# Optimization experiments

Hardware: AMD Instinct MI355X
Metric: run time of the kernel (lower is better)

## Reference

```python
import jax, jax.numpy as jnp
import numpy as np

NUM_EXPERTS = 8
TOP_K = 2


def setup_inputs() -> dict:
    key = jax.random.key(0)
    k0, k1, k2, k3, k4 = jax.random.split(key, 5)
    sl, bs, hs, ffn = 2048, 2, 512, 2048
    T = sl * bs
    x = jax.random.normal(k0, (sl, bs, hs), jnp.float32)
    expert_weights = jax.random.uniform(k1, (T, TOP_K), jnp.float32)
    expert_indices = jax.random.randint(k2, (T, TOP_K), 0, NUM_EXPERTS)
    # per-expert MLP params (ParallelGroupedMLP, 'regular' mlp_type)
    w1 = jax.random.normal(k3, (NUM_EXPERTS, hs, ffn), jnp.float32) * (hs ** -0.5)
    w2 = jax.random.normal(k4, (NUM_EXPERTS, ffn, hs), jnp.float32) * (ffn ** -0.5)
    return dict(x=x, expert_weights=expert_weights, expert_indices=expert_indices, w1=w1, w2=w2)


def reference(x, expert_weights, expert_indices, w1, w2):
    """Dropless MoE: sort assignments by expert, gather tokens, grouped MLP,
    scatter-combine with top-k router weights (megablocks gather/scatter semantics)."""
    in_shape = x.shape
    hs = in_shape[-1]
    x_flat = x.reshape(-1, hs)                 # [T, hs]
    T = x_flat.shape[0]
    flat_ids = expert_indices.reshape(-1)      # [T*k] expert id per assignment
    order = jnp.argsort(flat_ids)              # indices: assignment order sorted by expert
    bin_ids = flat_ids[order]                  # expert id per sorted slot
    token_ids = order // TOP_K                 # source token per sorted slot
    xg = x_flat[token_ids]                     # gather: [T*k, hs]
    # grouped GEMM: fixed small loop over experts, mask-select per slot
    y = jnp.zeros_like(xg)
    for e in range(NUM_EXPERTS):
        h = jax.nn.gelu(xg @ w1[e], approximate=False)   # [T*k, ffn]
        y = jnp.where((bin_ids == e)[:, None], h @ w2[e], y)
    # scatter-combine: out[token] += weight[assignment] * y[slot]
    w = expert_weights.reshape(-1)[order][:, None]       # [T*k, 1]
    out = jnp.zeros((T, hs), x.dtype).at[token_ids].add(w * y)
    return out.reshape(in_shape)
```

## Files before the change

kernel.cpp:

```cpp
#include <hip/hip_runtime.h>
#include <stdint.h>

#define T_TOK 4096
#define KTOP  2
#define HS    512
#define FFN   2048
#define NE    8
#define NA    (T_TOK*KTOP)
#define MT    128
#define BK    64
#define MT_MAX 72
#define SLOT_CAP (MT_MAX*MT)
#define PSTR 68
#define CPAD 32

#define MB_ (1024ull*1024ull)
#define WS_CNT2  0u
#define WS_OFF   1024u
#define WS_MEXP  1088u
#define WS_SLOTS 2048u
#define WS_INV   40960u
#define WS_XB   (1*MB_)
#define WS_W1T  (5*MB_)
#define WS_W2T  (21*MB_)
#define WS_HB   (37*MB_)
#define WS_YPB0 (73*MB_)
#define WS_YPB1 (82*MB_)
#define WS_NEED (91*MB_)

typedef short bf16x8 __attribute__((ext_vector_type(8)));
typedef float f32x4  __attribute__((ext_vector_type(4)));

__device__ __forceinline__ unsigned short f2bf(float f) {
    unsigned u = __builtin_bit_cast(unsigned, f);
    u += 0x7fffu + ((u >> 16) & 1u);
    return (unsigned short)(u >> 16);
}
__device__ __forceinline__ float bf2f(unsigned short h) {
    return __builtin_bit_cast(float, (unsigned)h << 16);
}
__device__ __forceinline__ float gelu_fast(float x) {
    float x2 = x * x;
    float inner = fmaf(0.044715f * x2, x, x);
    float E = __expf(1.5957691216057308f * inner);
    return x - x / (1.0f + E);
}
__device__ __forceinline__ void gl_lds16(const void* g, void* l) {
    __builtin_amdgcn_global_load_lds(
        (const __attribute__((address_space(1))) unsigned int*)g,
        (__attribute__((address_space(3))) unsigned int*)l, 16, 0, 0);
}

__device__ __forceinline__ void transpose_cvt_body(
    const float* __restrict__ src, unsigned short* __restrict__ dh,
    int R, int C, int e, int kb, int nb, int t, float (*tile)[33])
{
    const int k0 = kb * 32, n0 = nb * 32;
    #pragma unroll
    for (int q = 0; q < 4; ++q) {
        int idx = t + q * 256, kk = idx >> 5, nn = idx & 31;
        tile[kk][nn] = src[((size_t)e * R + k0 + kk) * C + n0 + nn];
    }
    __syncthreads();
    #pragma unroll
    for (int q = 0; q < 4; ++q) {
        int idx = t + q * 256, nn = idx >> 5, kk = idx & 31;
        dh[((size_t)e * C + n0 + nn) * R + k0 + kk] = f2bf(tile[kk][nn]);
    }
}

__global__ void moe_prep(int* slots, int* cnt2,
                         const float* __restrict__ x, unsigned short* __restrict__ xb,
                         const float* __restrict__ w1, unsigned short* __restrict__ w1t,
                         const float* __restrict__ w2, unsigned short* __restrict__ w2t)
{
    __shared__ float tile[32][33];
    const int bid = blockIdx.x, t = threadIdx.x;
    if (bid < 2048) {
        int i = bid * 256 + t;
        float4 v = reinterpret_cast<const float4*>(x)[i];
        uint2 p = { (unsigned)f2bf(v.x) | ((unsigned)f2bf(v.y) << 16),
                    (unsigned)f2bf(v.z) | ((unsigned)f2bf(v.w) << 16) };
        reinterpret_cast<uint2*>(xb)[i] = p;
    } else if (bid < 10240) {
        int lin = bid - 2048, e = lin >> 10, rem = lin & 1023;
        transpose_cvt_body(w1, w1t, HS, FFN, e, rem & 15, rem >> 4, t, tile);
    } else if (bid < 18432) {
        int lin = bid - 10240, e = lin >> 10, rem = lin & 1023;
        transpose_cvt_body(w2, w2t, FFN, HS, e, rem & 63, rem >> 6, t, tile);
    } else {
        int gid = (bid - 18432) * 256 + t;
        if (gid < SLOT_CAP) slots[gid] = -1;
        if (gid < NE * CPAD) cnt2[gid] = 0;
    }
}

__global__ void moe_fill(const int* __restrict__ eidx, int* cnt2, int* slots, int* inv,
                         int* offp, int* mexp) {
    __shared__ int h[NE];
    __shared__ int hloc[NE];
    __shared__ int bl[NE];
    __shared__ int off_l[NE + 1];
    const int t = threadIdx.x;
    if (t < NE) { h[t] = 0; hloc[t] = 0; }
    __syncthreads();
    for (int a2 = t; a2 < NA; a2 += 256) atomicAdd(&h[eidx[a2]], 1);
    const int a = blockIdx.x * 256 + t;
    const int e = eidx[a];
    const int rank = atomicAdd(&hloc[e], 1);
    __syncthreads();
    if (t == 0) {
        int run = 0;
        for (int q = 0; q < NE; ++q) { off_l[q] = run; run += ((h[q] + MT - 1) / MT) * MT; }
        off_l[NE] = run;
    }
    __syncthreads();
    if (t < NE) bl[t] = atomicAdd(&cnt2[t * CPAD], hloc[t]);
    if (blockIdx.x == 0) {
        if (t <= NE) offp[t] = off_l[t];
        if (t < MT_MAX) {
            int m0 = t * MT, ee = 0;
            #pragma unroll
            for (int q = 0; q < NE; ++q)
                if (m0 >= off_l[q] && m0 < off_l[q + 1]) ee = q;
            mexp[t] = ee;
        }
    }
    __syncthreads();
    int s = off_l[e] + bl[e] + rank;
    slots[s] = a;
    inv[a] = s;
}

__global__ __launch_bounds__(256, 4) void moe_gemm1(
    const unsigned short* __restrict__ XB, const unsigned short* __restrict__ W1T,
    const int* __restrict__ offp, const int* __restrict__ mexp,
    const int* __restrict__ slots, unsigned short* __restrict__ HB)
{
    const int xcd = blockIdx.x & 7;
    const int part = blockIdx.x >> 3;
    const int mtg = part % 9;
    const int nt  = part / 9;
    const int mt  = xcd * 9 + mtg;
    if (mt * MT >= offp[NE]) return;
    const int e = mexp[mt];
    const int t = threadIdx.x, lane = t & 63, wv = t >> 6;

    __shared__ __align__(16) char POOL[MT * PSTR * 4];
    __shared__ int srow[MT];
    short* As = (short*)POOL;
    short* Bs = (short*)(POOL + 16384);
    float* Pf = (float*)POOL;

    if (t < MT) { int s = slots[mt * MT + t]; srow[t] = (s < 0) ? 0 : (s >> 1); }
    __syncthreads();

    int baseA[4], baseB[4];
    #pragma unroll
    for (int q = 0; q < 4; ++q) {
        int i = wv * 4 + q;
        int row = i * 8 + (lane >> 3);
        int sg = (lane & 7) ^ (row & 7);
        baseA[q] = srow[row] * HS + sg * 8;
        baseB[q] = (e * FFN + nt * MT + row) * HS + sg * 8;
    }

    const int wm = wv >> 1, wn = wv & 1, q4 = lane >> 4, l15 = lane & 15;
    int offA[2][4], offB[2][4];
    #pragma unroll
    for (int m = 0; m < 4; ++m) {
        int r  = wm * 64 + m * 16 + l15;
        int rb = wn * 64 + m * 16 + l15;
        #pragma unroll
        for (int ks = 0; ks < 2; ++ks) {
            offA[ks][m] = r  * 128 + ((((ks << 2) | q4) ^ (r  & 7)) << 4);
            offB[ks][m] = rb * 128 + ((((ks << 2) | q4) ^ (rb & 7)) << 4);
        }
    }

    f32x4 acc[4][4];
    #pragma unroll
    for (int m = 0; m < 4; ++m)
        #pragma unroll
        for (int n = 0; n < 4; ++n) { f32x4 z = {0.f, 0.f, 0.f, 0.f}; acc[m][n] = z; }

    for (int kk = 0; kk < HS; kk += BK) {
        __syncthreads();
        #pragma unroll
        for (int q = 0; q < 4; ++q) {
            int i = wv * 4 + q;
            gl_lds16(XB  + baseA[q] + kk, (char*)As + i * 1024);
            gl_lds16(W1T + baseB[q] + kk, (char*)Bs + i * 1024);
        }
        __syncthreads();
        #pragma unroll
        for (int ks = 0; ks < 2; ++ks) {
            bf16x8 a[4], b[4];
            #pragma unroll
            for (int m = 0; m < 4; ++m) {
                a[m] = *(const bf16x8*)((const char*)As + offA[ks][m]);
                b[m] = *(const bf16x8*)((const char*)Bs + offB[ks][m]);
            }
            #pragma unroll
            for (int m = 0; m < 4; ++m)
                #pragma unroll
                for (int n = 0; n < 4; ++n)
                    acc[m][n] = __builtin_amdgcn_mfma_f32_16x16x32_bf16(a[m], b[n], acc[m][n], 0, 0, 0);
        }
    }

    #pragma unroll
    for (int half = 0; half < 2; ++half) {
        __syncthreads();
        if (wn == half) {
            #pragma unroll
            for (int m = 0; m < 4; ++m)
                #pragma unroll
                for (int n = 0; n < 4; ++n)
                    #pragma unroll
                    for (int j = 0; j < 4; ++j)
                        Pf[(wm * 64 + m * 16 + q4 * 4 + j) * PSTR + n * 16 + l15] = acc[m][n][j];
        }
        __syncthreads();
        #pragma unroll
        for (int q = 0; q < 4; ++q) {
            int seg = q * 256 + t, row = seg >> 3, c8 = (seg & 7) << 3;
            const float* p = Pf + row * PSTR + c8;
            float4 a = *(const float4*)p, b = *(const float4*)(p + 4);
            float va[8] = {a.x, a.y, a.z, a.w, b.x, b.y, b.z, b.w};
            bf16x8 ph;
            #pragma unroll
            for (int i = 0; i < 8; ++i) ph[i] = (short)f2bf(gelu_fast(va[i]));
            *(bf16x8*)(HB + (size_t)(mt * MT + row) * FFN + nt * MT + half * 64 + c8) = ph;
        }
    }
}

__global__ __launch_bounds__(256, 4) void moe_gemm2(
    const unsigned short* __restrict__ HB, const unsigned short* __restrict__ W2T,
    const int* __restrict__ offp, const int* __restrict__ mexp,
    unsigned short* __restrict__ YPB0, unsigned short* __restrict__ YPB1)
{
    const int xcd = blockIdx.x & 7;
    const int part = blockIdx.x >> 3;
    const int mtg = part % 9;
    const int sub = part / 9;
    const int mt  = xcd * 9 + mtg;
    const int nt  = sub >> 1, kpart = sub & 1;
    if (mt * MT >= offp[NE]) return;
    const int e = mexp[mt];
    const int t = threadIdx.x, lane = t & 63, wv = t >> 6;

    __shared__ __align__(16) char POOL[MT * PSTR * 4];
    short* As = (short*)POOL;
    short* Bs = (short*)(POOL + 16384);
    float* Pf = (float*)POOL;

    int baseA[4], baseB[4];
    #pragma unroll
    for (int q = 0; q < 4; ++q) {
        int i = wv * 4 + q;
        int row = i * 8 + (lane >> 3);
        int sg = (lane & 7) ^ (row & 7);
        baseA[q] = (mt * MT + row) * FFN + sg * 8;
        baseB[q] = (e * HS + nt * MT + row) * FFN + sg * 8;
    }

    const int wm = wv >> 1, wn = wv & 1, q4 = lane >> 4, l15 = lane & 15;
    int offA[2][4], offB[2][4];
    #pragma unroll
    for (int m = 0; m < 4; ++m) {
        int r  = wm * 64 + m * 16 + l15;
        int rb = wn * 64 + m * 16 + l15;
        #pragma unroll
        for (int ks = 0; ks < 2; ++ks) {
            offA[ks][m] = r  * 128 + ((((ks << 2) | q4) ^ (r  & 7)) << 4);
            offB[ks][m] = rb * 128 + ((((ks << 2) | q4) ^ (rb & 7)) << 4);
        }
    }

    f32x4 acc[4][4];
    #pragma unroll
    for (int m = 0; m < 4; ++m)
        #pragma unroll
        for (int n = 0; n < 4; ++n) { f32x4 z = {0.f, 0.f, 0.f, 0.f}; acc[m][n] = z; }

    const int k0 = kpart * (FFN / 2), k1 = k0 + FFN / 2;
    for (int kk = k0; kk < k1; kk += BK) {
        __syncthreads();
        #pragma unroll
        for (int q = 0; q < 4; ++q) {
            int i = wv * 4 + q;
            gl_lds16(HB  + baseA[q] + kk, (char*)As + i * 1024);
            gl_lds16(W2T + baseB[q] + kk, (char*)Bs + i * 1024);
        }
        __syncthreads();
        #pragma unroll
        for (int ks = 0; ks < 2; ++ks) {
            bf16x8 a[4], b[4];
            #pragma unroll
            for (int m = 0; m < 4; ++m) {
                a[m] = *(const bf16x8*)((const char*)As + offA[ks][m]);
                b[m] = *(const bf16x8*)((const char*)Bs + offB[ks][m]);
            }
            #pragma unroll
            for (int m = 0; m < 4; ++m)
                #pragma unroll
                for (int n = 0; n < 4; ++n)
                    acc[m][n] = __builtin_amdgcn_mfma_f32_16x16x32_bf16(a[m], b[n], acc[m][n], 0, 0, 0);
        }
    }

    unsigned short* YP = kpart ? YPB1 : YPB0;
    #pragma unroll
    for (int half = 0; half < 2; ++half) {
        __syncthreads();
        if (wn == half) {
            #pragma unroll
            for (int m = 0; m < 4; ++m)
                #pragma unroll
                for (int n = 0; n < 4; ++n)
                    #pragma unroll
                    for (int j = 0; j < 4; ++j)
                        Pf[(wm * 64 + m * 16 + q4 * 4 + j) * PSTR + n * 16 + l15] = acc[m][n][j];
        }
        __syncthreads();
        #pragma unroll
        for (int q = 0; q < 4; ++q) {
            int seg = q * 256 + t, row = seg >> 3, c8 = (seg & 7) << 3;
            const float* p = Pf + row * PSTR + c8;
            float4 a = *(const float4*)p, b = *(const float4*)(p + 4);
            float va[8] = {a.x, a.y, a.z, a.w, b.x, b.y, b.z, b.w};
            bf16x8 ph;
            #pragma unroll
            for (int i = 0; i < 8; ++i) ph[i] = (short)f2bf(va[i]);
            *(bf16x8*)(YP + (size_t)(mt * MT + row) * HS + nt * MT + half * 64 + c8) = ph;
        }
    }
}

__global__ void moe_combine2(const unsigned short* __restrict__ YPB0,
                             const unsigned short* __restrict__ YPB1,
                             const int* __restrict__ inv, const float* __restrict__ ew,
                             float* __restrict__ out) {
    int i = blockIdx.x * 256 + threadIdx.x;
    if (i >= T_TOK * HS / 8) return;
    int tk = i >> 6, c8 = (i & 63) << 3;
    int s0 = inv[2 * tk], s1 = inv[2 * tk + 1];
    float w0 = ew[2 * tk], w1 = ew[2 * tk + 1];
    bf16x8 a0 = *(const bf16x8*)(YPB0 + (size_t)s0 * HS + c8);
    bf16x8 b0 = *(const bf16x8*)(YPB1 + (size_t)s0 * HS + c8);
    bf16x8 a1 = *(const bf16x8*)(YPB0 + (size_t)s1 * HS + c8);
    bf16x8 b1 = *(const bf16x8*)(YPB1 + (size_t)s1 * HS + c8);
    float o[8];
    #pragma unroll
    for (int j = 0; j < 8; ++j)
        o[j] = w0 * (bf2f((unsigned short)a0[j]) + bf2f((unsigned short)b0[j]))
             + w1 * (bf2f((unsigned short)a1[j]) + bf2f((unsigned short)b1[j]));
    float4* d = reinterpret_cast<float4*>(out + (size_t)i * 8);
    d[0] = make_float4(o[0], o[1], o[2], o[3]);
    d[1] = make_float4(o[4], o[5], o[6], o[7]);
}

#define FB_BM 32
#define FB_BJ 128
#define FB_CK 256
#define FB_XSTR (FB_CK+4)
#define FB_HSTR (FB_BJ+4)

__device__ __forceinline__ float fb_gelu(float v) {
    return 0.5f * v * (1.0f + erff(v * 0.70710678118654752f));
}

__global__ void fb_init(int* cnt) { int i = threadIdx.x; if (i < NE) cnt[i] = 0; }

__global__ void fb_scatter(const int* __restrict__ eidx, int* cnt, int* bucket) {
    int a = blockIdx.x * 256 + threadIdx.x;
    if (a < NA) { int e = eidx[a]; int p = atomicAdd(&cnt[e], 1); bucket[e * NA + p] = a; }
}

__global__ __launch_bounds__(256, 1) void fb_fused(
    const float* __restrict__ x, const float* __restrict__ w1, const float* __restrict__ w2,
    const int* __restrict__ cnt, const int* __restrict__ bucket, float* __restrict__ ybuf)
{
    const int bid = blockIdx.x;
    const int e = bid & (NE - 1), tr = bid >> 3;
    const int n_e = cnt[e], rbase = tr * FB_BM;
    if (rbase >= n_e) return;
    const int t = threadIdx.x;
    __shared__ __align__(16) float Xc[FB_BM][FB_XSTR];
    __shared__ __align__(16) float Hsh[FB_BM][FB_HSTR];
    __shared__ int rowa[FB_BM];
    if (t < FB_BM) { int r = rbase + t; rowa[t] = (r < n_e) ? bucket[e * NA + r] : -1; }
    __syncthreads();
    const int cg = t & 15, rg = t >> 4, r0 = rg * 2;
    float yac[2][32];
    #pragma unroll
    for (int u = 0; u < 2; ++u)
        #pragma unroll
        for (int v = 0; v < 32; ++v) yac[u][v] = 0.0f;
    const float* w1e = w1 + (size_t)e * HS * FFN;
    const float* w2e = w2 + (size_t)e * FFN * HS;
    for (int jp = 0; jp < FFN; jp += FB_BJ) {
        float hac[2][8];
        #pragma unroll
        for (int u = 0; u < 2; ++u)
            #pragma unroll
            for (int v = 0; v < 8; ++v) hac[u][v] = 0.0f;
        for (int ic = 0; ic < HS; ic += FB_CK) {
            __syncthreads();
            #pragma unroll
            for (int q = 0; q < (FB_BM * FB_CK / 4) / 256; ++q) {
                int id = t + 256 * q, rr = id >> 6, c4 = id & 63;
                int a = rowa[rr];
                float4 val = make_float4(0.f, 0.f, 0.f, 0.f);
                if (a >= 0) val = *reinterpret_cast<const float4*>(x + (size_t)(a >> 1) * HS + ic + c4 * 4);
                *reinterpret_cast<float4*>(&Xc[rr][c4 * 4]) = val;
            }
            __syncthreads();
            const float* w1p = w1e + (size_t)ic * FFN + jp + cg * 8;
            #pragma unroll 2
            for (int i4 = 0; i4 < FB_CK; i4 += 4) {
                float4 xa = *reinterpret_cast<const float4*>(&Xc[r0][i4]);
                float4 xb = *reinterpret_cast<const float4*>(&Xc[r0 + 1][i4]);
                const float* wr0 = w1p + (size_t)i4 * FFN;
                #pragma unroll
                for (int ii = 0; ii < 4; ++ii) {
                    float4 wa = *reinterpret_cast<const float4*>(wr0 + (size_t)ii * FFN);
                    float4 wb = *reinterpret_cast<const float4*>(wr0 + (size_t)ii * FFN + 4);
                    float x0 = (ii == 0) ? xa.x : (ii == 1) ? xa.y : (ii == 2) ? xa.z : xa.w;
                    float x1 = (ii == 0) ? xb.x : (ii == 1) ? xb.y : (ii == 2) ? xb.z : xb.w;
                    hac[0][0] = fmaf(x0, wa.x, hac[0][0]); hac[0][1] = fmaf(x0, wa.y, hac[0][1]);
                    hac[0][2] = fmaf(x0, wa.z, hac[0][2]); hac[0][3] = fmaf(x0, wa.w, hac[0][3]);
                    hac[0][4] = fmaf(x0, wb.x, hac[0][4]); hac[0][5] = fmaf(x0, wb.y, hac[0][5]);
                    hac[0][6] = fmaf(x0, wb.z, hac[0][6]); hac[0][7] = fmaf(x0, wb.w, hac[0][7]);
                    hac[1][0] = fmaf(x1, wa.x, hac[1][0]); hac[1][1] = fmaf(x1, wa.y, hac[1][1]);
                    hac[1][2] = fmaf(x1, wa.z, hac[1][2]); hac[1][3] = fmaf(x1, wa.w, hac[1][3]);
                    hac[1][4] = fmaf(x1, wb.x, hac[1][4]); hac[1][5] = fmaf(x1, wb.y, hac[1][5]);
                    hac[1][6] = fmaf(x1, wb.z, hac[1][6]); hac[1][7] = fmaf(x1, wb.w, hac[1][7]);
                }
            }
        }
        #pragma unroll
        for (int u = 0; u < 2; ++u)
            #pragma unroll
            for (int v = 0; v < 8; ++v) Hsh[r0 + u][cg * 8 + v] = fb_gelu(hac[u][v]);
        __syncthreads();
        const float* w2p = w2e + (size_t)jp * HS + cg * 32;
        #pragma unroll 2
        for (int j = 0; j < FB_BJ; ++j) {
            float h0 = Hsh[r0][j], h1 = Hsh[r0 + 1][j];
            const float* wr = w2p + (size_t)j * HS;
            #pragma unroll
            for (int q = 0; q < 8; ++q) {
                float4 w4 = *reinterpret_cast<const float4*>(wr + q * 4);
                yac[0][q * 4 + 0] = fmaf(h0, w4.x, yac[0][q * 4 + 0]);
                yac[0][q * 4 + 1] = fmaf(h0, w4.y, yac[0][q * 4 + 1]);
                yac[0][q * 4 + 2] = fmaf(h0, w4.z, yac[0][q * 4 + 2]);
                yac[0][q * 4 + 3] = fmaf(h0, w4.w, yac[0][q * 4 + 3]);
                yac[1][q * 4 + 0] = fmaf(h1, w4.x, yac[1][q * 4 + 0]);
                yac[1][q * 4 + 1] = fmaf(h1, w4.y, yac[1][q * 4 + 1]);
                yac[1][q * 4 + 2] = fmaf(h1, w4.z, yac[1][q * 4 + 2]);
                yac[1][q * 4 + 3] = fmaf(h1, w4.w, yac[1][q * 4 + 3]);
            }
        }
    }
    #pragma unroll
    for (int u = 0; u < 2; ++u) {
        int a = rowa[r0 + u];
        if (a >= 0) {
            float* yp = ybuf + (size_t)a * HS + cg * 32;
            #pragma unroll
            for (int q = 0; q < 8; ++q) {
                float4 o = make_float4(yac[u][q * 4 + 0], yac[u][q * 4 + 1],
                                       yac[u][q * 4 + 2], yac[u][q * 4 + 3]);
                *reinterpret_cast<float4*>(yp + q * 4) = o;
            }
        }
    }
}

__global__ void fb_combine(const float* __restrict__ ybuf, const float* __restrict__ ew,
                           float* __restrict__ out) {
    int i = blockIdx.x * 256 + threadIdx.x;
    if (i >= T_TOK * HS / 4) return;
    int tk = i >> 7, c4 = i & 127;
    float wA = ew[2 * tk], wB = ew[2 * tk + 1];
    const float4* y4 = reinterpret_cast<const float4*>(ybuf);
    float4 a = y4[(size_t)(2 * tk) * (HS / 4) + c4];
    float4 b = y4[(size_t)(2 * tk + 1) * (HS / 4) + c4];
    float4 o;
    o.x = wA * a.x + wB * b.x; o.y = wA * a.y + wB * b.y;
    o.z = wA * a.z + wB * b.z; o.w = wA * a.w + wB * b.w;
    reinterpret_cast<float4*>(out)[i] = o;
}

extern "C" void kernel_launch(void* const* d_in, const int* in_sizes, int n_in,
                              void* d_out, int out_size, void* d_ws, size_t ws_size,
                              hipStream_t stream) {
    const float* x  = (const float*)d_in[0];
    const float* ew = (const float*)d_in[1];
    const int*   ei = (const int*)d_in[2];
    const float* w1 = (const float*)d_in[3];
    const float* w2 = (const float*)d_in[4];
    float* out = (float*)d_out;
    char* W = (char*)d_ws;

    if (ws_size < WS_NEED) {
        int* cnt = (int*)d_ws;
        int* bucket = cnt + 64;
        float* ybuf = (float*)(W + (1 << 19));
        fb_init<<<1, 64, 0, stream>>>(cnt);
        fb_scatter<<<NA / 256, 256, 0, stream>>>(ei, cnt, bucket);
        fb_fused<<<NE * (NA / FB_BM), 256, 0, stream>>>(x, w1, w2, cnt, bucket, ybuf);
        fb_combine<<<(T_TOK * HS / 4 + 255) / 256, 256, 0, stream>>>(ybuf, ew, out);
        return;
    }

    int* cnt2  = (int*)(W + WS_CNT2);
    int* offp  = (int*)(W + WS_OFF);
    int* mexp  = (int*)(W + WS_MEXP);
    int* slots = (int*)(W + WS_SLOTS);
    int* inv   = (int*)(W + WS_INV);
    unsigned short* XB   = (unsigned short*)(W + WS_XB);
    unsigned short* W1T  = (unsigned short*)(W + WS_W1T);
    unsigned short* W2T  = (unsigned short*)(W + WS_W2T);
    unsigned short* HB   = (unsigned short*)(W + WS_HB);
    unsigned short* YPB0 = (unsigned short*)(W + WS_YPB0);
    unsigned short* YPB1 = (unsigned short*)(W + WS_YPB1);

    moe_prep<<<18468, 256, 0, stream>>>(slots, cnt2, x, XB, w1, W1T, w2, W2T);
    moe_fill<<<NA / 256, 256, 0, stream>>>(ei, cnt2, slots, inv, offp, mexp);
    moe_gemm1<<<8 * 9 * 16, 256, 0, stream>>>(XB, W1T, offp, mexp, slots, HB);
    moe_gemm2<<<8 * 9 * 8, 256, 0, stream>>>(HB, W2T, offp, mexp, YPB0, YPB1);
    moe_combine2<<<(T_TOK * HS / 8) / 256, 256, 0, stream>>>(YPB0, YPB1, inv, ew, out);
}
```

Baseline: 101.5 us.

## Fuse routing fill into prep kernel with deterministic prefix-based slot ranks

Merges the separate routing-fill kernel into the prep kernel, so there is one fewer launch and no global atomic counter to zero. Each routing block recomputes the full histogram plus a prefix histogram of all earlier assignments and takes ranks by a linear scan, which makes slot order deterministic. One extra block pads only the unused slots and writes the offsets and expert map. The gemm2 block-to-tile mapping is also reordered so consecutive blocks share the same M tile. The cost is that each of 33 blocks scans all 8192 expert ids and runs an O(t) rank loop.

Result: no change. 101.2 us (-0.2%).

```diff
diff --git a/kernel.cpp b/kernel.cpp
--- a/kernel.cpp
+++ b/kernel.cpp
@@ -12,10 +12,8 @@
 #define MT_MAX 72
 #define SLOT_CAP (MT_MAX*MT)
 #define PSTR 68
-#define CPAD 32
 
 #define MB_ (1024ull*1024ull)
-#define WS_CNT2  0u
 #define WS_OFF   1024u
 #define WS_MEXP  1088u
 #define WS_SLOTS 2048u
@@ -69,7 +67,8 @@
     }
 }
 
-__global__ void moe_prep(int* slots, int* cnt2,
+__global__ void moe_prep(const int* __restrict__ eidx,
+                         int* slots, int* inv, int* offp, int* mexp,
                          const float* __restrict__ x, unsigned short* __restrict__ xb,
                          const float* __restrict__ w1, unsigned short* __restrict__ w1t,
                          const float* __restrict__ w2, unsigned short* __restrict__ w2t)
@@ -89,47 +88,47 @@
         int lin = bid - 10240, e = lin >> 10, rem = lin & 1023;
         transpose_cvt_body(w2, w2t, FFN, HS, e, rem & 63, rem >> 6, t, tile);
     } else {
-        int gid = (bid - 18432) * 256 + t;
-        if (gid < SLOT_CAP) slots[gid] = -1;
-        if (gid < NE * CPAD) cnt2[gid] = 0;
-    }
-}
-
-__global__ void moe_fill(const int* __restrict__ eidx, int* cnt2, int* slots, int* inv,
-                         int* offp, int* mexp) {
-    __shared__ int h[NE];
-    __shared__ int hloc[NE];
-    __shared__ int bl[NE];
-    __shared__ int off_l[NE + 1];
-    const int t = threadIdx.x;
-    if (t < NE) { h[t] = 0; hloc[t] = 0; }
-    __syncthreads();
-    for (int a2 = t; a2 < NA; a2 += 256) atomicAdd(&h[eidx[a2]], 1);
-    const int a = blockIdx.x * 256 + t;
-    const int e = eidx[a];
-    const int rank = atomicAdd(&hloc[e], 1);
-    __syncthreads();
-    if (t == 0) {
-        int run = 0;
-        for (int q = 0; q < NE; ++q) { off_l[q] = run; run += ((h[q] + MT - 1) / MT) * MT; }
-        off_l[NE] = run;
-    }
-    __syncthreads();
-    if (t < NE) bl[t] = atomicAdd(&cnt2[t * CPAD], hloc[t]);
-    if (blockIdx.x == 0) {
-        if (t <= NE) offp[t] = off_l[t];
-        if (t < MT_MAX) {
-            int m0 = t * MT, ee = 0;
-            #pragma unroll
-            for (int q = 0; q < NE; ++q)
-                if (m0 >= off_l[q] && m0 < off_l[q + 1]) ee = q;
-            mexp[t] = ee;
-        }
-    }
-    __syncthreads();
-    int s = off_l[e] + bl[e] + rank;
-    slots[s] = a;
-    inv[a] = s;
+        __shared__ int hfull[NE], hpre[NE], elocal[256];
+        __shared__ int off_l[NE + 1];
+        const int f = bid - 18432;
+        if (t < NE) { hfull[t] = 0; hpre[t] = 0; }
+        __syncthreads();
+        const int base = f * 256;
+        for (int i = t; i < NA; i += 256) {
+            int ee = eidx[i];
+            atomicAdd(&hfull[ee], 1);
+            if (i < base) atomicAdd(&hpre[ee], 1);
+        }
+        if (f < 32) elocal[t] = eidx[base + t];
+        __syncthreads();
+        if (t == 0) {
+            int run = 0;
+            for (int q = 0; q < NE; ++q) { off_l[q] = run; run += ((hfull[q] + MT - 1) / MT) * MT; }
+            off_l[NE] = run;
+        }
+        __syncthreads();
+        if (f < 32) {
+            int a = base + t, e = elocal[t];
+            int rank = 0;
+            for (int j = 0; j < t; ++j) rank += (elocal[j] == e) ? 1 : 0;
+            int s = off_l[e] + hpre[e] + rank;
+            slots[s] = a;
+            inv[a] = s;
+        } else {
+            for (int e = 0; e < NE; ++e)
+                for (int s = off_l[e] + hfull[e] + t; s < off_l[e + 1]; s += 256)
+                    slots[s] = -1;
+            for (int s = off_l[NE] + t; s < SLOT_CAP; s += 256) slots[s] = -1;
+            if (t <= NE) offp[t] = off_l[t];
+            if (t < MT_MAX) {
+                int m0 = t * MT, ee = 0;
+                #pragma unroll
+                for (int q = 0; q < NE; ++q)
+                    if (m0 >= off_l[q] && m0 < off_l[q + 1]) ee = q;
+                mexp[t] = ee;
+            }
+        }
+    }
 }
 
 __global__ __launch_bounds__(256, 4) void moe_gemm1(
@@ -243,8 +242,8 @@
 {
     const int xcd = blockIdx.x & 7;
     const int part = blockIdx.x >> 3;
-    const int mtg = part % 9;
-    const int sub = part / 9;
+    const int sub = part % 8;
+    const int mtg = part / 8;
     const int mt  = xcd * 9 + mtg;
     const int nt  = sub >> 1, kpart = sub & 1;
     if (mt * MT >= offp[NE]) return;
@@ -517,7 +516,6 @@
         return;
     }
 
-    int* cnt2  = (int*)(W + WS_CNT2);
     int* offp  = (int*)(W + WS_OFF);
     int* mexp  = (int*)(W + WS_MEXP);
     int* slots = (int*)(W + WS_SLOTS);
@@ -529,8 +527,8 @@
     unsigned short* YPB0 = (unsigned short*)(W + WS_YPB0);
     unsigned short* YPB1 = (unsigned short*)(W + WS_YPB1);
 
-    moe_prep<<<18468, 256, 0, stream>>>(slots, cnt2, x, XB, w1, W1T, w2, W2T);
-    moe_fill<<<NA / 256, 256, 0, stream>>>(ei, cnt2, slots, inv, offp, mexp);
+    moe_prep<<<18465, 256, 0, stream>>>(ei, slots, inv, offp, mexp,
+                                        x, XB, w1, W1T, w2, W2T);
     moe_gemm1<<<8 * 9 * 16, 256, 0, stream>>>(XB, W1T, offp, mexp, slots, HB);
     moe_gemm2<<<8 * 9 * 8, 256, 0, stream>>>(HB, W2T, offp, mexp, YPB0, YPB1);
     moe_combine2<<<(T_TOK * HS / 8) / 256, 256, 0, stream>>>(YPB0, YPB1, inv, ew, out);
```
